# Kernel optimization log

Measured on AMD Instinct MI355X. Metric: run time of the kernel, lower is better.

The kernel has to match this reference:

```python
import jax, jax.numpy as jnp
import numpy as np

NEG_INF = -1e30


def setup_inputs() -> dict:
    key = jax.random.key(0)
    ks = jax.random.split(key, 11)
    b, n, d = 4, 2048, 1024
    scale = 1.0 / np.sqrt(d)
    inp = {
        "q": jax.random.normal(ks[0], (b, n, d), jnp.float32),
        "k": jax.random.normal(ks[1], (b, n, d), jnp.float32),
        "v": jax.random.normal(ks[2], (b, n, d), jnp.float32),
        # nn.Linear params: weight [out, in], bias [out]
        "Wq": jax.random.normal(ks[3], (d, d), jnp.float32) * scale,
        "bq": jnp.zeros((d,), jnp.float32),
        "Wk": jax.random.normal(ks[4], (d, d), jnp.float32) * scale,
        "bk": jnp.zeros((d,), jnp.float32),
        "Wv": jax.random.normal(ks[5], (d, d), jnp.float32) * scale,
        "bv": jnp.zeros((d,), jnp.float32),
        "Wo": jax.random.normal(ks[6], (d, d), jnp.float32) * scale,
        "bo": jnp.zeros((d,), jnp.float32),
    }
    return inp


def reference(q, k, v, Wq, bq, Wk, bk, Wv, bv, Wo, bo):
    # Faithful to source: the multi-head reshape/transpose results are never
    # assigned, so attention runs single-headed over full n_embd vectors.
    b, n, d = q.shape
    qp = q @ Wq.T + bq  # [b, n, d]
    kp = k @ Wk.T + bk
    vp = v @ Wv.T + bv
    scale = jnp.asarray(1.0 / d, qp.dtype) ** 0.5  # sqrt(1/d)
    att = jnp.einsum('bnd,bmd->bnm', qp, kp) * scale  # [b, n, n]
    causal = jnp.tril(jnp.ones((n, n), bool))          # block_size tril sliced to n
    att = jnp.where(causal[None, :, :], att, NEG_INF)
    att = jax.nn.softmax(att, axis=-1)  # dropout p=0.0 -> identity
    y = att @ vp                        # [b, n, d]
    # source bug reproduced: transpose(1,2) then reshape(b, n, d)
    y = jnp.swapaxes(y, 1, 2).reshape(b, n, d)
    y = y @ Wo.T + bo
    return y
```

## Files before the change

### kernel.cpp

```cpp
#include <hip/hip_runtime.h>
#include <hip/hip_bf16.h>
#include <stdint.h>

typedef __bf16 bf16_t;
typedef __bf16 bf16x8 __attribute__((ext_vector_type(8)));
typedef __bf16 bf16x4 __attribute__((ext_vector_type(4)));
typedef float f32x4 __attribute__((ext_vector_type(4)));

#define GLD_LDS16(src, dst)                                                              \
  __builtin_amdgcn_global_load_lds((const __attribute__((address_space(1))) void*)(src), \
                                   (__attribute__((address_space(3))) void*)(dst), 16, 0, 0)

#define BAR() __builtin_amdgcn_s_barrier()
#define LGKM0() asm volatile("s_waitcnt lgkmcnt(0)" ::: "memory")
#define VMCN(n) asm volatile("s_waitcnt vmcnt(" #n ")" ::: "memory")
#define SCH0() __builtin_amdgcn_sched_barrier(0)

__device__ __forceinline__ int swz(int x) { return x ^ (((x >> 9) & 1) << 5); }

struct CvtArgs {
  const float* src[7];
  bf16_t* dst[7];
  long n4[7];
};

__global__ __launch_bounds__(256) void cvt_all(CvtArgs a) {
  const int seg = blockIdx.y;
  const float* __restrict__ in = a.src[seg];
  bf16_t* __restrict__ out = a.dst[seg];
  const long n4 = a.n4[seg];
  long i = (long)blockIdx.x * blockDim.x + threadIdx.x;
  const long stride = (long)gridDim.x * blockDim.x;
  for (; i < n4; i += stride) {
    float4 v = ((const float4*)in)[i];
    bf16x4 o;
    o[0] = (bf16_t)v.x; o[1] = (bf16_t)v.y; o[2] = (bf16_t)v.z; o[3] = (bf16_t)v.w;
    ((bf16x4*)out)[i] = o;
  }
}

__global__ __launch_bounds__(256) void softmax_causal(bf16_t* __restrict__ S, int n, long sB) {
  const int i = blockIdx.x;
  const int z = blockIdx.y;
  bf16_t* row = S + (long)z * sB + (long)i * n;
  const int t = threadIdx.x;
  const int j0 = t << 3;

  bf16x8 vv = ((const bf16x8*)row)[t];
  float vals[8];
  float mx = -3.0e38f;
#pragma unroll
  for (int e = 0; e < 8; ++e) {
    float v = (j0 + e <= i) ? (float)vv[e] : -3.0e38f;
    vals[e] = v;
    mx = fmaxf(mx, v);
  }
#pragma unroll
  for (int off = 32; off; off >>= 1) mx = fmaxf(mx, __shfl_xor(mx, off));
  __shared__ float redm[4];
  if ((t & 63) == 0) redm[t >> 6] = mx;
  __syncthreads();
  mx = fmaxf(fmaxf(redm[0], redm[1]), fmaxf(redm[2], redm[3]));

  float sum = 0.f;
#pragma unroll
  for (int e = 0; e < 8; ++e) {
    float p = (j0 + e <= i) ? __expf(vals[e] - mx) : 0.f;
    vals[e] = p;
    sum += p;
  }
#pragma unroll
  for (int off = 32; off; off >>= 1) sum += __shfl_xor(sum, off);
  __shared__ float reds[4];
  if ((t & 63) == 0) reds[t >> 6] = sum;
  __syncthreads();
  sum = reds[0] + reds[1] + reds[2] + reds[3];
  const float inv = 1.0f / sum;

  bf16x8 o;
#pragma unroll
  for (int e = 0; e < 8; ++e) o[e] = (bf16_t)(vals[e] * inv);
  ((bf16x8*)row)[t] = o;
}

__device__ __forceinline__ void xcd_remap(int& bx, int& by, int& bz) {
  const int gx = gridDim.x, gy = gridDim.y;
  int lin = (blockIdx.z * gy + blockIdx.y) * gx + blockIdx.x;
  const int nwg = gx * gy * (int)gridDim.z;
  lin = (lin & 7) * (nwg >> 3) + (lin >> 3);
  bx = lin % gx;
  const int rem = lin / gx;
  by = rem % gy;
  bz = rem / gy;
}

struct G8Args {
  const bf16_t* A[3];
  const bf16_t* W[3];
  const float* bias[3];
  bf16_t* C[3];
  long sA, sB, sC;
};

template <int HALF, int BUF>
__device__ __forceinline__ void stage8(char* lds, const bf16_t* srcH, const int (&soff)[2],
                                       int wid, int tile) {
  const bf16_t* s = srcH + tile * 64;
  char* d = lds + (HALF >= 2 ? 65536 : 0) + BUF * 32768 + (HALF & 1) * 16384 + wid * 2048;
  GLD_LDS16(s + soff[0], d);
  GLD_LDS16(s + soff[1], d + 1024);
}

template <int BUF, int QM>
__device__ __forceinline__ void rdA(char* lds, const int (&aoffp)[4][2], bf16x8 (&af)[4][2]) {
  char* b = lds + BUF * 32768 + QM * 16384;
#pragma unroll
  for (int mi = 0; mi < 4; ++mi)
#pragma unroll
    for (int kk = 0; kk < 2; ++kk) af[mi][kk] = *(const bf16x8*)(b + aoffp[mi][kk]);
}

template <int BUF, int QN>
__device__ __forceinline__ void rdB(char* lds, const int (&boffp)[2][2], bf16x8 (&bf)[2][2]) {
  char* b = lds + 65536 + BUF * 32768 + QN * 16384;
#pragma unroll
  for (int ni = 0; ni < 2; ++ni)
#pragma unroll
    for (int kk = 0; kk < 2; ++kk) bf[ni][kk] = *(const bf16x8*)(b + boffp[ni][kk]);
}

template <int QM, int QN>
__device__ __forceinline__ void mm16(f32x4 (&acc)[2][2][4][2], const bf16x8 (&af)[4][2],
                                     const bf16x8 (&bf)[2][2]) {
  __builtin_amdgcn_s_setprio(1);
#pragma unroll
  for (int mi = 0; mi < 4; ++mi)
#pragma unroll
    for (int ni = 0; ni < 2; ++ni)
#pragma unroll
      for (int kk = 0; kk < 2; ++kk)
        acc[QM][QN][mi][ni] = __builtin_amdgcn_mfma_f32_16x16x32_bf16(
            af[mi][kk], bf[ni][kk], acc[QM][QN][mi][ni], 0, 0, 0);
  __builtin_amdgcn_s_setprio(0);
}

template <bool LAST>
__device__ __forceinline__ void kiter(char* lds, int tt,
    const bf16_t* srcA0, const bf16_t* srcA1, const bf16_t* srcB0, const bf16_t* srcB1,
    const int (&soff)[2], int wid,
    const int (&aoffp)[4][2], const int (&boffp)[2][2],
    bf16x8 (&af)[4][2], bf16x8 (&bf0)[2][2], bf16x8 (&bf1)[2][2],
    f32x4 (&acc)[2][2][4][2]) {
  VMCN(8); LGKM0(); SCH0();
  mm16<0, 0>(acc, af, bf0);
  rdB<0, 1>(lds, boffp, bf1);
  stage8<1, 1>(lds, srcA1, soff, wid, tt + 1);
  SCH0(); BAR();
  VMCN(8); LGKM0(); SCH0();
  mm16<0, 1>(acc, af, bf1);
  rdA<0, 1>(lds, aoffp, af);
  if (!LAST) stage8<0, 0>(lds, srcA0, soff, wid, tt + 2);
  SCH0(); BAR();
  if (LAST) { VMCN(0); } else { VMCN(6); }
  LGKM0(); SCH0();
  mm16<1, 0>(acc, af, bf0);
  rdB<1, 0>(lds, boffp, bf0);
  if (!LAST) stage8<2, 0>(lds, srcB0, soff, wid, tt + 2);
  SCH0(); BAR();
  LGKM0(); SCH0();
  mm16<1, 1>(acc, af, bf1);
  rdA<1, 0>(lds, aoffp, af);
  if (!LAST) stage8<3, 0>(lds, srcB1, soff, wid, tt + 2);
  SCH0(); BAR();
  if (!LAST) { VMCN(8); }
  LGKM0(); SCH0();
  mm16<0, 0>(acc, af, bf0);
  rdB<1, 1>(lds, boffp, bf1);
  if (!LAST) stage8<1, 0>(lds, srcA1, soff, wid, tt + 2);
  SCH0(); BAR();
  if (!LAST) { VMCN(8); }
  LGKM0(); SCH0();
  mm16<0, 1>(acc, af, bf1);
  rdA<1, 1>(lds, aoffp, af);
  if (!LAST) stage8<0, 1>(lds, srcA0, soff, wid, tt + 3);
  SCH0(); BAR();
  if (!LAST) { VMCN(6); }
  LGKM0(); SCH0();
  mm16<1, 0>(acc, af, bf0);
  if (!LAST) rdB<0, 0>(lds, boffp, bf0);
  if (!LAST) stage8<2, 1>(lds, srcB0, soff, wid, tt + 3);
  SCH0(); BAR();
  LGKM0(); SCH0();
  mm16<1, 1>(acc, af, bf1);
  if (!LAST) rdA<0, 0>(lds, aoffp, af);
  if (!LAST) stage8<3, 1>(lds, srcB1, soff, wid, tt + 3);
  SCH0(); BAR();
}

template <int MODE>
__global__ __launch_bounds__(512, 2) void gemm8(G8Args ga) {
  int bx, by, bz;
  xcd_remap(bx, by, bz);
  const int m0 = by << 8, n0 = bx << 8;
  if (MODE == 1 && n0 > m0 + 255) return;

  const int K = 1024, NT = 16;
  const bf16_t* A;
  const bf16_t* B;
  const float* bias = nullptr;
  if (MODE == 0) {
    A = ga.A[bz]; B = ga.W[bz]; bias = ga.bias[bz];
  } else {
    A = ga.A[0] + (long)bz * ga.sA;
    B = ga.W[0] + (long)bz * ga.sB;
  }

  __shared__ __align__(16) char lds[131072];

  const int t = threadIdx.x;
  const int wid = t >> 6, l = t & 63;
  const int wm = wid >> 2, wn = wid & 3;
  const int ri16 = l & 15, kg = l >> 4;

  int soff[2];
#pragma unroll
  for (int i = 0; i < 2; ++i) {
    const int sub = wid * 2 + i;
    const int ri = l >> 2;
    const int cq = (l & 3) ^ ((ri & 8) >> 2);
    const int r = (sub >> 1) * 16 + ri;
    const int c = (sub & 1) * 32 + cq * 8;
    soff[i] = r * K + c;
  }
  const bf16_t* srcA0 = A + (long)m0 * K;
  const bf16_t* srcA1 = A + (long)(m0 + 128) * K;
  const bf16_t* srcB0 = B + (long)n0 * K;
  const bf16_t* srcB1 = B + (long)(n0 + 128) * K;

  int aoffp[4][2], boffp[2][2];
#pragma unroll
  for (int mi = 0; mi < 4; ++mi)
#pragma unroll
    for (int kk = 0; kk < 2; ++kk)
      aoffp[mi][kk] = swz((wm * 4 + mi) * 2048 + kk * 1024 + ri16 * 64 + kg * 16);
#pragma unroll
  for (int ni = 0; ni < 2; ++ni)
#pragma unroll
    for (int kk = 0; kk < 2; ++kk)
      boffp[ni][kk] = swz((wn * 2 + ni) * 2048 + kk * 1024 + ri16 * 64 + kg * 16);

  f32x4 acc[2][2][4][2] = {};
  bf16x8 af[4][2], bf0[2][2], bf1[2][2];

  stage8<0, 0>(lds, srcA0, soff, wid, 0);
  stage8<2, 0>(lds, srcB0, soff, wid, 0);
  stage8<3, 0>(lds, srcB1, soff, wid, 0);
  stage8<1, 0>(lds, srcA1, soff, wid, 0);
  stage8<0, 1>(lds, srcA0, soff, wid, 1);
  stage8<2, 1>(lds, srcB0, soff, wid, 1);
  stage8<3, 1>(lds, srcB1, soff, wid, 1);
  VMCN(6);
  BAR();
  rdA<0, 0>(lds, aoffp, af);
  rdB<0, 0>(lds, boffp, bf0);

  for (int tt = 0; tt + 2 < NT; tt += 2)
    kiter<false>(lds, tt, srcA0, srcA1, srcB0, srcB1, soff, wid, aoffp, boffp,
                 af, bf0, bf1, acc);
  kiter<true>(lds, NT - 2, srcA0, srcA1, srcB0, srcB1, soff, wid, aoffp, boffp,
              af, bf0, bf1, acc);

  if (MODE == 0) {
    if (bz < 2) {
      bf16_t* C = ga.C[bz];
#pragma unroll
      for (int qm = 0; qm < 2; ++qm)
#pragma unroll
        for (int qn = 0; qn < 2; ++qn)
#pragma unroll
          for (int mi = 0; mi < 4; ++mi)
#pragma unroll
            for (int ni = 0; ni < 2; ++ni) {
              const int col = n0 + qn * 128 + wn * 32 + ni * 16 + ri16;
              const int row0 = m0 + qm * 128 + wm * 64 + mi * 16 + kg * 4;
              const float badd = bias[col];
#pragma unroll
              for (int j = 0; j < 4; ++j)
                C[(long)(row0 + j) * 1024 + col] = (bf16_t)(acc[qm][qn][mi][ni][j] + badd);
            }
    } else {
      bf16_t* C = ga.C[2];
#pragma unroll
      for (int qm = 0; qm < 2; ++qm)
#pragma unroll
        for (int qn = 0; qn < 2; ++qn)
#pragma unroll
          for (int mi = 0; mi < 4; ++mi)
#pragma unroll
            for (int ni = 0; ni < 2; ++ni) {
              const int col = n0 + qn * 128 + wn * 32 + ni * 16 + ri16;
              const int row0 = m0 + qm * 128 + wm * 64 + mi * 16 + kg * 4;
              const float badd = bias[col];
              const int batch = row0 >> 11, nr = row0 & 2047;
              bf16x4 o;
#pragma unroll
              for (int j = 0; j < 4; ++j) o[j] = (bf16_t)(acc[qm][qn][mi][ni][j] + badd);
              *(bf16x4*)(C + (long)batch * (2048 * 1024) + (long)col * 2048 + nr) = o;
            }
    }
  } else {
    bf16_t* C = ga.C[0] + (long)bz * ga.sC;
#pragma unroll
    for (int qm = 0; qm < 2; ++qm)
#pragma unroll
      for (int qn = 0; qn < 2; ++qn)
#pragma unroll
        for (int mi = 0; mi < 4; ++mi)
#pragma unroll
          for (int ni = 0; ni < 2; ++ni) {
            const int col = n0 + qn * 128 + wn * 32 + ni * 16 + ri16;
            const int row0 = m0 + qm * 128 + wm * 64 + mi * 16 + kg * 4;
#pragma unroll
            for (int j = 0; j < 4; ++j)
              C[(long)(row0 + j) * 2048 + col] = (bf16_t)(acc[qm][qn][mi][ni][j] * 0.03125f);
          }
  }
}

template <bool BF16_OUT, bool BIAS, bool KBOUND>
__device__ __forceinline__ void gemm_body(const bf16_t* __restrict__ A,
                                          const bf16_t* __restrict__ B,
                                          const float* __restrict__ bias,
                                          void* __restrict__ Cout,
                                          int N, int K, float alpha,
                                          int m0, int n0) {
  int KT = K >> 5;
  if (KBOUND) {
    int kb = (n0 + 128) >> 5;
    if (kb < KT) KT = kb;
  }

  __shared__ __align__(16) bf16_t As[128 * 32];
  __shared__ __align__(16) bf16_t Bs[128 * 32];

  const int t = threadIdx.x;
  const int l = t & 63;
  const int w = t >> 6;
  const int wr = w >> 1, wc = w & 1;

  const int c0 = t, c1 = t + 256;
  const bf16_t* a_src0 = A + (long)(m0 + (c0 >> 2)) * K + ((c0 & 3) << 3);
  const bf16_t* a_src1 = A + (long)(m0 + (c1 >> 2)) * K + ((c1 & 3) << 3);
  const bf16_t* b_src0 = B + (long)(n0 + (c0 >> 2)) * K + ((c0 & 3) << 3);
  const bf16_t* b_src1 = B + (long)(n0 + (c1 >> 2)) * K + ((c1 & 3) << 3);
  char* const asb = (char*)As;
  char* const bsb = (char*)Bs;
  char* const a_dst0 = asb + w * 1024;
  char* const a_dst1 = asb + 4096 + w * 1024;
  char* const b_dst0 = bsb + w * 1024;
  char* const b_dst1 = bsb + 4096 + w * 1024;

  const int r16 = l & 15, kg = l >> 4;
  int aoff[4], boff[4];
#pragma unroll
  for (int mi = 0; mi < 4; ++mi) aoff[mi] = (((wr * 64 + mi * 16 + r16) * 32) + kg * 8) * 2;
#pragma unroll
  for (int ni = 0; ni < 4; ++ni) boff[ni] = (((wc * 64 + ni * 16 + r16) * 32) + kg * 8) * 2;

  f32x4 acc[4][4] = {};

  for (int kt = 0; kt < KT; ++kt) {
    __syncthreads();
    GLD_LDS16(a_src0, a_dst0);
    GLD_LDS16(a_src1, a_dst1);
    GLD_LDS16(b_src0, b_dst0);
    GLD_LDS16(b_src1, b_dst1);
    a_src0 += 32; a_src1 += 32; b_src0 += 32; b_src1 += 32;
    __syncthreads();

    bf16x8 af[4], bfr[4];
#pragma unroll
    for (int mi = 0; mi < 4; ++mi) af[mi] = *(const bf16x8*)(asb + aoff[mi]);
#pragma unroll
    for (int ni = 0; ni < 4; ++ni) bfr[ni] = *(const bf16x8*)(bsb + boff[ni]);
#pragma unroll
    for (int mi = 0; mi < 4; ++mi)
#pragma unroll
      for (int ni = 0; ni < 4; ++ni)
        acc[mi][ni] = __builtin_amdgcn_mfma_f32_16x16x32_bf16(af[mi], bfr[ni], acc[mi][ni], 0, 0, 0);
  }

  const int rowbase = m0 + wr * 64 + ((l >> 4) << 2);
  const int colbase = n0 + wc * 64 + (l & 15);
  if constexpr (BF16_OUT) {
    bf16_t* C = (bf16_t*)Cout;
#pragma unroll
    for (int mi = 0; mi < 4; ++mi)
#pragma unroll
      for (int ni = 0; ni < 4; ++ni) {
        const int col = colbase + ni * 16;
        float badd = 0.f;
        if constexpr (BIAS) badd = bias[col];
#pragma unroll
        for (int j = 0; j < 4; ++j) {
          float v = acc[mi][ni][j] * alpha + badd;
          C[(long)(rowbase + mi * 16 + j) * N + col] = (bf16_t)v;
        }
      }
  } else {
    float* C = (float*)Cout;
#pragma unroll
    for (int mi = 0; mi < 4; ++mi)
#pragma unroll
      for (int ni = 0; ni < 4; ++ni) {
        const int col = colbase + ni * 16;
        float badd = 0.f;
        if constexpr (BIAS) badd = bias[col];
#pragma unroll
        for (int j = 0; j < 4; ++j) {
          float v = acc[mi][ni][j] * alpha + badd;
          C[(long)(rowbase + mi * 16 + j) * N + col] = v;
        }
      }
  }
}

template <bool BF16_OUT, bool BIAS, bool KBOUND>
__global__ __launch_bounds__(256, 4) void gemm_bt(const bf16_t* __restrict__ A,
                                                  const bf16_t* __restrict__ B,
                                                  const float* __restrict__ bias,
                                                  void* __restrict__ Cout,
                                                  int N, int K, float alpha,
                                                  long sAb, long sBb, long sCb, int eltC) {
  int bx, by, bz;
  xcd_remap(bx, by, bz);
  const int m0 = by << 7, n0 = bx << 7;
  gemm_body<BF16_OUT, BIAS, KBOUND>(A + (long)bz * sAb, B + (long)bz * sBb, bias,
                                    (char*)Cout + (long)bz * sCb * eltC, N, K, alpha, m0, n0);
}

extern "C" void kernel_launch(void* const* d_in, const int* in_sizes, int n_in,
                              void* d_out, int out_size, void* d_ws, size_t ws_size,
                              hipStream_t stream) {
  const int b = 4, n = 2048, d = 1024;
  const long nd  = (long)n * d;
  const long bn  = (long)b * n;
  const long bnd = bn * d;
  const long ddl = (long)d * d;
  const long nn  = (long)n * n;

  const float* q  = (const float*)d_in[0];
  const float* k  = (const float*)d_in[1];
  const float* v  = (const float*)d_in[2];
  const float* Wq = (const float*)d_in[3];
  const float* bq = (const float*)d_in[4];
  const float* Wk = (const float*)d_in[5];
  const float* bk = (const float*)d_in[6];
  const float* Wv = (const float*)d_in[7];
  const float* bv = (const float*)d_in[8];
  const float* Wo = (const float*)d_in[9];
  const float* bo = (const float*)d_in[10];

  bf16_t* ws  = (bf16_t*)d_ws;
  bf16_t* qB  = ws;
  bf16_t* kB  = qB + bnd;
  bf16_t* vB  = kB + bnd;
  bf16_t* WqB = vB + bnd;
  bf16_t* WkB = WqB + ddl;
  bf16_t* WvB = WkB + ddl;
  bf16_t* WoB = WvB + ddl;
  bf16_t* qpB = WoB + ddl;
  bf16_t* kpB = qpB + bnd;
  bf16_t* vpT = kpB + bnd;
  bf16_t* S   = vpT + bnd;
  bf16_t* yT  = S + (long)b * nn;
  const size_t need = (size_t)(7 * bnd + 4 * ddl + (long)b * nn) * 2;
  if (ws_size < need) return;

  dim3 blk(256);

  CvtArgs ca;
  ca.src[0] = q;  ca.dst[0] = qB;  ca.n4[0] = bnd / 4;
  ca.src[1] = k;  ca.dst[1] = kB;  ca.n4[1] = bnd / 4;
  ca.src[2] = v;  ca.dst[2] = vB;  ca.n4[2] = bnd / 4;
  ca.src[3] = Wq; ca.dst[3] = WqB; ca.n4[3] = ddl / 4;
  ca.src[4] = Wk; ca.dst[4] = WkB; ca.n4[4] = ddl / 4;
  ca.src[5] = Wv; ca.dst[5] = WvB; ca.n4[5] = ddl / 4;
  ca.src[6] = Wo; ca.dst[6] = WoB; ca.n4[6] = ddl / 4;
  cvt_all<<<dim3(512, 7), blk, 0, stream>>>(ca);

  G8Args qa = {};
  qa.A[0] = qB; qa.W[0] = WqB; qa.bias[0] = bq; qa.C[0] = qpB;
  qa.A[1] = kB; qa.W[1] = WkB; qa.bias[1] = bk; qa.C[1] = kpB;
  qa.A[2] = vB; qa.W[2] = WvB; qa.bias[2] = bv; qa.C[2] = vpT;
  gemm8<0><<<dim3(d / 256, bn / 256, 3), dim3(512), 0, stream>>>(qa);

  G8Args sa = {};
  sa.A[0] = qpB; sa.W[0] = kpB; sa.C[0] = S;
  sa.sA = nd; sa.sB = nd; sa.sC = nn;
  gemm8<1><<<dim3(n / 256, n / 256, b), dim3(512), 0, stream>>>(sa);

  softmax_causal<<<dim3(n, b), blk, 0, stream>>>(S, n, nn);

  gemm_bt<true, false, true><<<dim3(n / 128, d / 128, b), blk, 0, stream>>>(
      vpT, S, nullptr, yT, n, n, 1.f, nd, nn, nd, 2);

  gemm_bt<false, true, false><<<dim3(d / 128, bn / 128, 1), blk, 0, stream>>>(
      yT, WoB, bo, (float*)d_out, d, d, 1.f, 0, 0, 0, 4);
}
```

Before: 210.7 us.

## Fuse fp32-to-bf16 conversion of q/k/v into QKV projection GEMM; trim softmax work

Removes the separate conversion pass for the large q, k and v activations by reading fp32 directly in a new 128x128-tile QKV GEMM that converts to bf16 while staging into LDS. The highly tuned 256x256 pipelined gemm8 path is no longer used for the projections. It is replaced by a simpler single-buffered kernel with synchronous global loads and two barriers per k-step. The softmax also skips loading, computing and storing columns beyond the 128-aligned causal boundary. This saves a full fp32 read plus bf16 write round trip over q/k/v, but the projection GEMM may be less efficient and now reads fp32 A three times per tile column.

```diff
diff --git a/kernel.cpp b/kernel.cpp
--- a/kernel.cpp
+++ b/kernel.cpp
@@ -19,9 +19,9 @@
 __device__ __forceinline__ int swz(int x) { return x ^ (((x >> 9) & 1) << 5); }
 
 struct CvtArgs {
-  const float* src[7];
-  bf16_t* dst[7];
-  long n4[7];
+  const float* src[4];
+  bf16_t* dst[4];
+  long n4[4];
 };
 
 __global__ __launch_bounds__(256) void cvt_all(CvtArgs a) {
@@ -45,15 +45,19 @@
   bf16_t* row = S + (long)z * sB + (long)i * n;
   const int t = threadIdx.x;
   const int j0 = t << 3;
-
-  bf16x8 vv = ((const bf16x8*)row)[t];
+  const int jmax = ((i >> 7) + 1) << 7;
+  const bool active = j0 < jmax;
+
   float vals[8];
   float mx = -3.0e38f;
-#pragma unroll
-  for (int e = 0; e < 8; ++e) {
-    float v = (j0 + e <= i) ? (float)vv[e] : -3.0e38f;
-    vals[e] = v;
-    mx = fmaxf(mx, v);
+  if (active) {
+    bf16x8 vv = ((const bf16x8*)row)[t];
+#pragma unroll
+    for (int e = 0; e < 8; ++e) {
+      float v = (j0 + e <= i) ? (float)vv[e] : -3.0e38f;
+      vals[e] = v;
+      mx = fmaxf(mx, v);
+    }
   }
 #pragma unroll
   for (int off = 32; off; off >>= 1) mx = fmaxf(mx, __shfl_xor(mx, off));
@@ -63,11 +67,13 @@
   mx = fmaxf(fmaxf(redm[0], redm[1]), fmaxf(redm[2], redm[3]));
 
   float sum = 0.f;
-#pragma unroll
-  for (int e = 0; e < 8; ++e) {
-    float p = (j0 + e <= i) ? __expf(vals[e] - mx) : 0.f;
-    vals[e] = p;
-    sum += p;
+  if (active) {
+#pragma unroll
+    for (int e = 0; e < 8; ++e) {
+      float p = (j0 + e <= i) ? __expf(vals[e] - mx) : 0.f;
+      vals[e] = p;
+      sum += p;
+    }
   }
 #pragma unroll
   for (int off = 32; off; off >>= 1) sum += __shfl_xor(sum, off);
@@ -77,10 +83,12 @@
   sum = reds[0] + reds[1] + reds[2] + reds[3];
   const float inv = 1.0f / sum;
 
-  bf16x8 o;
-#pragma unroll
-  for (int e = 0; e < 8; ++e) o[e] = (bf16_t)(vals[e] * inv);
-  ((bf16x8*)row)[t] = o;
+  if (active) {
+    bf16x8 o;
+#pragma unroll
+    for (int e = 0; e < 8; ++e) o[e] = (bf16_t)(vals[e] * inv);
+    ((bf16x8*)row)[t] = o;
+  }
 }
 
 __device__ __forceinline__ void xcd_remap(int& bx, int& by, int& bz) {
@@ -205,15 +213,8 @@
   if (MODE == 1 && n0 > m0 + 255) return;
 
   const int K = 1024, NT = 16;
-  const bf16_t* A;
-  const bf16_t* B;
-  const float* bias = nullptr;
-  if (MODE == 0) {
-    A = ga.A[bz]; B = ga.W[bz]; bias = ga.bias[bz];
-  } else {
-    A = ga.A[0] + (long)bz * ga.sA;
-    B = ga.W[0] + (long)bz * ga.sB;
-  }
+  const bf16_t* A = ga.A[0] + (long)bz * ga.sA;
+  const bf16_t* B = ga.W[0] + (long)bz * ga.sB;
 
   __shared__ __align__(16) char lds[131072];
 
@@ -270,61 +271,21 @@
   kiter<true>(lds, NT - 2, srcA0, srcA1, srcB0, srcB1, soff, wid, aoffp, boffp,
               af, bf0, bf1, acc);
 
-  if (MODE == 0) {
-    if (bz < 2) {
-      bf16_t* C = ga.C[bz];
-#pragma unroll
-      for (int qm = 0; qm < 2; ++qm)
-#pragma unroll
-        for (int qn = 0; qn < 2; ++qn)
-#pragma unroll
-          for (int mi = 0; mi < 4; ++mi)
-#pragma unroll
-            for (int ni = 0; ni < 2; ++ni) {
-              const int col = n0 + qn * 128 + wn * 32 + ni * 16 + ri16;
-              const int row0 = m0 + qm * 128 + wm * 64 + mi * 16 + kg * 4;
-              const float badd = bias[col];
-#pragma unroll
-              for (int j = 0; j < 4; ++j)
-                C[(long)(row0 + j) * 1024 + col] = (bf16_t)(acc[qm][qn][mi][ni][j] + badd);
-            }
-    } else {
-      bf16_t* C = ga.C[2];
-#pragma unroll
-      for (int qm = 0; qm < 2; ++qm)
-#pragma unroll
-        for (int qn = 0; qn < 2; ++qn)
-#pragma unroll
-          for (int mi = 0; mi < 4; ++mi)
-#pragma unroll
-            for (int ni = 0; ni < 2; ++ni) {
-              const int col = n0 + qn * 128 + wn * 32 + ni * 16 + ri16;
-              const int row0 = m0 + qm * 128 + wm * 64 + mi * 16 + kg * 4;
-              const float badd = bias[col];
-              const int batch = row0 >> 11, nr = row0 & 2047;
-              bf16x4 o;
-#pragma unroll
-              for (int j = 0; j < 4; ++j) o[j] = (bf16_t)(acc[qm][qn][mi][ni][j] + badd);
-              *(bf16x4*)(C + (long)batch * (2048 * 1024) + (long)col * 2048 + nr) = o;
-            }
-    }
-  } else {
-    bf16_t* C = ga.C[0] + (long)bz * ga.sC;
-#pragma unroll
-    for (int qm = 0; qm < 2; ++qm)
-#pragma unroll
-      for (int qn = 0; qn < 2; ++qn)
-#pragma unroll
-        for (int mi = 0; mi < 4; ++mi)
-#pragma unroll
-          for (int ni = 0; ni < 2; ++ni) {
-            const int col = n0 + qn * 128 + wn * 32 + ni * 16 + ri16;
-            const int row0 = m0 + qm * 128 + wm * 64 + mi * 16 + kg * 4;
-#pragma unroll
-            for (int j = 0; j < 4; ++j)
-              C[(long)(row0 + j) * 2048 + col] = (bf16_t)(acc[qm][qn][mi][ni][j] * 0.03125f);
-          }
-  }
+  bf16_t* C = ga.C[0] + (long)bz * ga.sC;
+#pragma unroll
+  for (int qm = 0; qm < 2; ++qm)
+#pragma unroll
+    for (int qn = 0; qn < 2; ++qn)
+#pragma unroll
+      for (int mi = 0; mi < 4; ++mi)
+#pragma unroll
+        for (int ni = 0; ni < 2; ++ni) {
+          const int col = n0 + qn * 128 + wn * 32 + ni * 16 + ri16;
+          const int row0 = m0 + qm * 128 + wm * 64 + mi * 16 + kg * 4;
+#pragma unroll
+          for (int j = 0; j < 4; ++j)
+            C[(long)(row0 + j) * 2048 + col] = (bf16_t)(acc[qm][qn][mi][ni][j] * 0.03125f);
+        }
 }
 
 template <bool BF16_OUT, bool BIAS, bool KBOUND>
@@ -439,6 +400,113 @@
                                     (char*)Cout + (long)bz * sCb * eltC, N, K, alpha, m0, n0);
 }
 
+struct QkvArgsF {
+  const float* A[3];
+  const bf16_t* W[3];
+  const float* bias[3];
+  bf16_t* C[3];
+};
+
+__global__ __launch_bounds__(256, 4) void gemm_qkv_f32a(QkvArgsF ga, int N, int K) {
+  int bx, by, bz;
+  xcd_remap(bx, by, bz);
+  const int m0 = by << 7, n0 = bx << 7;
+
+  const float* __restrict__ A = ga.A[bz];
+  const bf16_t* __restrict__ B = ga.W[bz];
+  const float* __restrict__ bias = ga.bias[bz];
+
+  const int KT = K >> 5;
+
+  __shared__ __align__(16) bf16_t As[128 * 32];
+  __shared__ __align__(16) bf16_t Bs[128 * 32];
+
+  const int t = threadIdx.x;
+  const int l = t & 63;
+  const int w = t >> 6;
+  const int wr = w >> 1, wc = w & 1;
+
+  const int c0 = t, c1 = t + 256;
+  const float* a_src0 = A + (long)(m0 + (c0 >> 2)) * K + ((c0 & 3) << 3);
+  const float* a_src1 = A + (long)(m0 + (c1 >> 2)) * K + ((c1 & 3) << 3);
+  const bf16_t* b_src0 = B + (long)(n0 + (c0 >> 2)) * K + ((c0 & 3) << 3);
+  const bf16_t* b_src1 = B + (long)(n0 + (c1 >> 2)) * K + ((c1 & 3) << 3);
+  char* const asb = (char*)As;
+  char* const bsb = (char*)Bs;
+  char* const b_dst0 = bsb + w * 1024;
+  char* const b_dst1 = bsb + 4096 + w * 1024;
+
+  const int r16 = l & 15, kg = l >> 4;
+  int aoff[4], boff[4];
+#pragma unroll
+  for (int mi = 0; mi < 4; ++mi) aoff[mi] = (((wr * 64 + mi * 16 + r16) * 32) + kg * 8) * 2;
+#pragma unroll
+  for (int ni = 0; ni < 4; ++ni) boff[ni] = (((wc * 64 + ni * 16 + r16) * 32) + kg * 8) * 2;
+
+  f32x4 acc[4][4] = {};
+
+  for (int kt = 0; kt < KT; ++kt) {
+    __syncthreads();
+    float4 x0 = *(const float4*)(a_src0);
+    float4 x1 = *(const float4*)(a_src0 + 4);
+    float4 y0 = *(const float4*)(a_src1);
+    float4 y1 = *(const float4*)(a_src1 + 4);
+    GLD_LDS16(b_src0, b_dst0);
+    GLD_LDS16(b_src1, b_dst1);
+    bf16x8 wa, wb;
+    wa[0] = (bf16_t)x0.x; wa[1] = (bf16_t)x0.y; wa[2] = (bf16_t)x0.z; wa[3] = (bf16_t)x0.w;
+    wa[4] = (bf16_t)x1.x; wa[5] = (bf16_t)x1.y; wa[6] = (bf16_t)x1.z; wa[7] = (bf16_t)x1.w;
+    wb[0] = (bf16_t)y0.x; wb[1] = (bf16_t)y0.y; wb[2] = (bf16_t)y0.z; wb[3] = (bf16_t)y0.w;
+    wb[4] = (bf16_t)y1.x; wb[5] = (bf16_t)y1.y; wb[6] = (bf16_t)y1.z; wb[7] = (bf16_t)y1.w;
+    *(bf16x8*)(asb + c0 * 16) = wa;
+    *(bf16x8*)(asb + c1 * 16) = wb;
+    a_src0 += 32; a_src1 += 32; b_src0 += 32; b_src1 += 32;
+    __syncthreads();
+
+    bf16x8 af[4], bfr[4];
+#pragma unroll
+    for (int mi = 0; mi < 4; ++mi) af[mi] = *(const bf16x8*)(asb + aoff[mi]);
+#pragma unroll
+    for (int ni = 0; ni < 4; ++ni) bfr[ni] = *(const bf16x8*)(bsb + boff[ni]);
+#pragma unroll
+    for (int mi = 0; mi < 4; ++mi)
+#pragma unroll
+      for (int ni = 0; ni < 4; ++ni)
+        acc[mi][ni] = __builtin_amdgcn_mfma_f32_16x16x32_bf16(af[mi], bfr[ni], acc[mi][ni], 0, 0, 0);
+  }
+
+  const int rowbase = m0 + wr * 64 + ((l >> 4) << 2);
+  const int colbase = n0 + wc * 64 + (l & 15);
+  if (bz < 2) {
+    bf16_t* C = ga.C[bz];
+#pragma unroll
+    for (int mi = 0; mi < 4; ++mi)
+#pragma unroll
+      for (int ni = 0; ni < 4; ++ni) {
+        const int col = colbase + ni * 16;
+        const float badd = bias[col];
+#pragma unroll
+        for (int j = 0; j < 4; ++j)
+          C[(long)(rowbase + mi * 16 + j) * N + col] = (bf16_t)(acc[mi][ni][j] + badd);
+      }
+  } else {
+    bf16_t* C = ga.C[2];
+#pragma unroll
+    for (int mi = 0; mi < 4; ++mi)
+#pragma unroll
+      for (int ni = 0; ni < 4; ++ni) {
+        const int col = colbase + ni * 16;
+        const float badd = bias[col];
+        const int row0 = rowbase + mi * 16;
+        const int batch = row0 >> 11, nr = row0 & 2047;
+        bf16x4 o;
+#pragma unroll
+        for (int j = 0; j < 4; ++j) o[j] = (bf16_t)(acc[mi][ni][j] + badd);
+        *(bf16x4*)(C + (long)batch * (2048 * 1024) + (long)col * 2048 + nr) = o;
+      }
+  }
+}
+
 extern "C" void kernel_launch(void* const* d_in, const int* in_sizes, int n_in,
                               void* d_out, int out_size, void* d_ws, size_t ws_size,
                               hipStream_t stream) {
@@ -462,10 +530,7 @@
   const float* bo = (const float*)d_in[10];
 
   bf16_t* ws  = (bf16_t*)d_ws;
-  bf16_t* qB  = ws;
-  bf16_t* kB  = qB + bnd;
-  bf16_t* vB  = kB + bnd;
-  bf16_t* WqB = vB + bnd;
+  bf16_t* WqB = ws;
   bf16_t* WkB = WqB + ddl;
   bf16_t* WvB = WkB + ddl;
   bf16_t* WoB = WvB + ddl;
@@ -474,26 +539,23 @@
   bf16_t* vpT = kpB + bnd;
   bf16_t* S   = vpT + bnd;
   bf16_t* yT  = S + (long)b * nn;
-  const size_t need = (size_t)(7 * bnd + 4 * ddl + (long)b * nn) * 2;
+  const size_t need = (size_t)(4 * ddl + 4 * bnd + (long)b * nn) * 2;
   if (ws_size < need) return;
 
   dim3 blk(256);
 
   CvtArgs ca;
-  ca.src[0] = q;  ca.dst[0] = qB;  ca.n4[0] = bnd / 4;
-  ca.src[1] = k;  ca.dst[1] = kB;  ca.n4[1] = bnd / 4;
-  ca.src[2] = v;  ca.dst[2] = vB;  ca.n4[2] = bnd / 4;
-  ca.src[3] = Wq; ca.dst[3] = WqB; ca.n4[3] = ddl / 4;
-  ca.src[4] = Wk; ca.dst[4] = WkB; ca.n4[4] = ddl / 4;
-  ca.src[5] = Wv; ca.dst[5] = WvB; ca.n4[5] = ddl / 4;
-  ca.src[6] = Wo; ca.dst[6] = WoB; ca.n4[6] = ddl / 4;
-  cvt_all<<<dim3(512, 7), blk, 0, stream>>>(ca);
-
-  G8Args qa = {};
-  qa.A[0] = qB; qa.W[0] = WqB; qa.bias[0] = bq; qa.C[0] = qpB;
-  qa.A[1] = kB; qa.W[1] = WkB; qa.bias[1] = bk; qa.C[1] = kpB;
-  qa.A[2] = vB; qa.W[2] = WvB; qa.bias[2] = bv; qa.C[2] = vpT;
-  gemm8<0><<<dim3(d / 256, bn / 256, 3), dim3(512), 0, stream>>>(qa);
+  ca.src[0] = Wq; ca.dst[0] = WqB; ca.n4[0] = ddl / 4;
+  ca.src[1] = Wk; ca.dst[1] = WkB; ca.n4[1] = ddl / 4;
+  ca.src[2] = Wv; ca.dst[2] = WvB; ca.n4[2] = ddl / 4;
+  ca.src[3] = Wo; ca.dst[3] = WoB; ca.n4[3] = ddl / 4;
+  cvt_all<<<dim3(256, 4), blk, 0, stream>>>(ca);
+
+  QkvArgsF qa;
+  qa.A[0] = q; qa.W[0] = WqB; qa.bias[0] = bq; qa.C[0] = qpB;
+  qa.A[1] = k; qa.W[1] = WkB; qa.bias[1] = bk; qa.C[1] = kpB;
+  qa.A[2] = v; qa.W[2] = WvB; qa.bias[2] = bv; qa.C[2] = vpT;
+  gemm_qkv_f32a<<<dim3(d / 128, bn / 128, 3), blk, 0, stream>>>(qa, d, d);
 
   G8Args sa = {};
   sa.A[0] = qpB; sa.W[0] = kpB; sa.C[0] = S;
```

New measurement: 203.6 us. 1.03x faster.
